# Kernel optimization log

Measured on AMD Instinct MI355X. Metric: run time of the kernel, lower is better.

Reference implementation:

```python
import jax, jax.numpy as jnp
import numpy as np

N_FEATURES = 512
FEATURE_DIM = 768
HIDDEN_DIM = 256


def setup_inputs() -> dict:
    key = jax.random.key(0)
    k0, k1, k2 = jax.random.split(key, 3)
    feature_embeddings = jax.random.normal(k0, (N_FEATURES, FEATURE_DIM), dtype=jnp.float32)
    # Linear(feature_dim*2 -> hidden) params, PyTorch-style init scale
    W1 = jax.random.normal(k1, (2 * FEATURE_DIM, HIDDEN_DIM), dtype=jnp.float32) / np.sqrt(2 * FEATURE_DIM)
    b1 = jnp.zeros((HIDDEN_DIM,), dtype=jnp.float32)
    W2 = jax.random.normal(k2, (HIDDEN_DIM, 1), dtype=jnp.float32) / np.sqrt(HIDDEN_DIM)
    b2 = jnp.zeros((1,), dtype=jnp.float32)
    return {"feature_embeddings": feature_embeddings, "W1": W1, "b1": b1, "W2": W2, "b2": b2}


def reference(feature_embeddings, W1, b1, W2, b2):
    n = feature_embeddings.shape[0]
    # all (i, j) with i < j -- same order as the original nested loop
    i_idx, j_idx = jnp.triu_indices(n, k=1)          # [P], [P]
    pairs = jnp.concatenate(
        [feature_embeddings[i_idx], feature_embeddings[j_idx]], axis=-1
    )                                                 # [P, 2*feature_dim]
    h = jax.nn.relu(pairs @ W1 + b1)                  # [P, hidden]
    scores = h @ W2 + b2                              # [P, 1]
    return i_idx, j_idx, scores
```

## Files before the change

### kernel.cpp

```cpp
#include <hip/hip_runtime.h>

#define FD 768
#define HD 256
#define NF 512
#define NC 512
#define PAIRS (NF * (NF - 1) / 2)

typedef __attribute__((ext_vector_type(4))) float f32x4;
typedef __attribute__((ext_vector_type(8))) short bf16x8;

__device__ inline unsigned bf16pk(float a, float b) {
    unsigned ua = __float_as_uint(a), ub = __float_as_uint(b);
    ua = (ua + 0x7FFFu + ((ua >> 16) & 1u)) >> 16;
    ub = (ub + 0x7FFFu + ((ub >> 16) & 1u)) >> 16;
    return ua | (ub << 16);
}

__global__ __launch_bounds__(256) void prep_kernel(
    const float* __restrict__ E, const float* __restrict__ W1,
    ushort* __restrict__ Ebf, ushort* __restrict__ Wt)
{
    const int bid = blockIdx.x, tid = threadIdx.x;
    if (bid < 384) {
        int idx = bid * 256 + tid;
        float4 v = ((const float4*)E)[idx];
        uint2 pk;
        pk.x = bf16pk(v.x, v.y);
        pk.y = bf16pk(v.z, v.w);
        *(uint2*)(Ebf + (size_t)idx * 4) = pk;
    } else {
        int t = (bid - 384) * 256 + tid;
        int q = t & 127, kp = t >> 7;
        int off = (q < 64) ? 0 : FD;
        int cq = q & 63;
        const float4* W14 = (const float4*)W1;
        float4 w0 = W14[(size_t)(2 * kp + off) * 64 + cq];
        float4 w1 = W14[(size_t)(2 * kp + 1 + off) * 64 + cq];
        *(unsigned*)(Wt + (size_t)(4 * q + 0) * FD + 2 * kp) = bf16pk(w0.x, w1.x);
        *(unsigned*)(Wt + (size_t)(4 * q + 1) * FD + 2 * kp) = bf16pk(w0.y, w1.y);
        *(unsigned*)(Wt + (size_t)(4 * q + 2) * FD + 2 * kp) = bf16pk(w0.z, w1.z);
        *(unsigned*)(Wt + (size_t)(4 * q + 3) * FD + 2 * kp) = bf16pk(w0.w, w1.w);
    }
}

__global__ __launch_bounds__(256) void gemm_mfma_kernel(
    const ushort* __restrict__ Ebf, const ushort* __restrict__ Wt,
    const float* __restrict__ b1, float* __restrict__ C)
{
    const int tid  = threadIdx.x;
    const int lane = tid & 63, wave = tid >> 6;
    const int wr = wave >> 1, wc = wave & 1;
    const int r0 = blockIdx.y * 32, c0 = blockIdx.x * 32;
    const int n = lane & 15, g = lane >> 4;

    const ushort* aptr = Wt  + (size_t)(c0 + 16 * wc + n) * FD + 8 * g;
    const ushort* bptr = Ebf + (size_t)(r0 + 16 * wr + n) * FD + 8 * g;

    f32x4 acc = {0.f, 0.f, 0.f, 0.f};
    #pragma unroll 8
    for (int ks = 0; ks < 24; ++ks) {
        bf16x8 af = *(const bf16x8*)(aptr + 32 * ks);
        bf16x8 bf = *(const bf16x8*)(bptr + 32 * ks);
        acc = __builtin_amdgcn_mfma_f32_16x16x32_bf16(af, bf, acc, 0, 0, 0);
    }

    const int row = r0 + 16 * wr + n;
    const int col = c0 + 16 * wc + 4 * g;
    float4 b = {0.f, 0.f, 0.f, 0.f};
    if (c0 < 256) b = ((const float4*)b1)[col >> 2];
    float4 o = {acc[0] + b.x, acc[1] + b.y, acc[2] + b.z, acc[3] + b.w};
    *(float4*)&C[(size_t)row * NC + col] = o;
}

__global__ __launch_bounds__(256) void pair_kernel(
    const float* __restrict__ C, const float* __restrict__ W2,
    const float* __restrict__ b2, float* __restrict__ out)
{
    __shared__ float4 As[16 * 64];
    __shared__ float4 Bs[32 * 64];

    int rem = blockIdx.x, bi = 0;
    while (rem >= 16 - (bi >> 1)) { rem -= 16 - (bi >> 1); ++bi; }
    const int bj = (bi >> 1) + rem;
    const int i0 = bi * 16, j0 = bj * 32;

    const int tid = threadIdx.x;
    const float4* C4 = (const float4*)C;

    #pragma unroll
    for (int s = 0; s < 4; ++s) {
        int idx = tid + 256 * s;
        int row = idx >> 6, c4 = idx & 63;
        As[row * 64 + (c4 ^ ((row >> 1) & 7))] = C4[(i0 + row) * 128 + c4];
    }
    #pragma unroll
    for (int s = 0; s < 8; ++s) {
        int idx = tid + 256 * s;
        int row = idx >> 6, c4 = idx & 63;
        Bs[row * 64 + (c4 ^ ((row >> 1) & 7))] = C4[(j0 + row) * 128 + 64 + c4];
    }
    __syncthreads();

    const int tx = tid & 15, ty = tid >> 4;
    const int keyA = (ty >> 1) & 7, keyB = tx & 7;
    const float4* W24 = (const float4*)W2;

    float acc0 = 0.f, acc1 = 0.f;
    #pragma unroll 8
    for (int k4 = 0; k4 < HD / 4; ++k4) {
        float4 a   = As[ty * 64 + (k4 ^ keyA)];
        float4 b0  = Bs[(2 * tx + 0) * 64 + (k4 ^ keyB)];
        float4 b1v = Bs[(2 * tx + 1) * 64 + (k4 ^ keyB)];
        float4 w = W24[k4];
        acc0 = fmaf(fmaxf(a.x + b0.x, 0.f), w.x, acc0);
        acc0 = fmaf(fmaxf(a.y + b0.y, 0.f), w.y, acc0);
        acc0 = fmaf(fmaxf(a.z + b0.z, 0.f), w.z, acc0);
        acc0 = fmaf(fmaxf(a.w + b0.w, 0.f), w.w, acc0);
        acc1 = fmaf(fmaxf(a.x + b1v.x, 0.f), w.x, acc1);
        acc1 = fmaf(fmaxf(a.y + b1v.y, 0.f), w.y, acc1);
        acc1 = fmaf(fmaxf(a.z + b1v.z, 0.f), w.z, acc1);
        acc1 = fmaf(fmaxf(a.w + b1v.w, 0.f), w.w, acc1);
    }

    const float bias2 = b2[0];
    const int i = i0 + ty;
    #pragma unroll
    for (int u = 0; u < 2; ++u) {
        int j = j0 + 2 * tx + u;
        float v = u ? acc1 : acc0;
        if (j > i) {
            int p = i * (2 * NF - i - 1) / 2 + (j - i - 1);
            out[p]             = (float)i;
            out[PAIRS + p]     = (float)j;
            out[2 * PAIRS + p] = v + bias2;
        }
    }
}

extern "C" void kernel_launch(void* const* d_in, const int* in_sizes, int n_in,
                              void* d_out, int out_size, void* d_ws, size_t ws_size,
                              hipStream_t stream) {
    const float* E  = (const float*)d_in[0];
    const float* W1 = (const float*)d_in[1];
    const float* b1 = (const float*)d_in[2];
    const float* W2 = (const float*)d_in[3];
    const float* b2 = (const float*)d_in[4];
    float* out = (float*)d_out;

    ushort* Ebf = (ushort*)d_ws;
    ushort* Wt  = Ebf + (size_t)NF * FD;
    float*  C   = (float*)((char*)d_ws + 2 * (size_t)NF * FD * 2);

    prep_kernel<<<576, 256, 0, stream>>>(E, W1, Ebf, Wt);
    gemm_mfma_kernel<<<dim3(16, 16), 256, 0, stream>>>(Ebf, Wt, b1, C);
    pair_kernel<<<272, 256, 0, stream>>>(C, W2, b2, out);
}
```

Baseline: 28.20 us.

## Transpose W1 via shared-memory tiles and compute 2x2 pairs per thread

The W1 transpose in the prep kernel now stages 64x64 tiles in padded shared memory, so both the global reads and the bf16 writes of the transposed weights are coalesced instead of strided. The pair kernel drops to 128 threads per block, each computing a 2x2 block of pair scores, which doubles register reuse of the A and B rows loaded from LDS. Fewer threads per block means less latency hiding and fewer waves per block across 272 blocks.

```diff
diff --git a/kernel.cpp b/kernel.cpp
--- a/kernel.cpp
+++ b/kernel.cpp
@@ -28,18 +28,40 @@
         pk.x = bf16pk(v.x, v.y);
         pk.y = bf16pk(v.z, v.w);
         *(uint2*)(Ebf + (size_t)idx * 4) = pk;
-    } else {
-        int t = (bid - 384) * 256 + tid;
-        int q = t & 127, kp = t >> 7;
-        int off = (q < 64) ? 0 : FD;
-        int cq = q & 63;
-        const float4* W14 = (const float4*)W1;
-        float4 w0 = W14[(size_t)(2 * kp + off) * 64 + cq];
-        float4 w1 = W14[(size_t)(2 * kp + 1 + off) * 64 + cq];
-        *(unsigned*)(Wt + (size_t)(4 * q + 0) * FD + 2 * kp) = bf16pk(w0.x, w1.x);
-        *(unsigned*)(Wt + (size_t)(4 * q + 1) * FD + 2 * kp) = bf16pk(w0.y, w1.y);
-        *(unsigned*)(Wt + (size_t)(4 * q + 2) * FD + 2 * kp) = bf16pk(w0.z, w1.z);
-        *(unsigned*)(Wt + (size_t)(4 * q + 3) * FD + 2 * kp) = bf16pk(w0.w, w1.w);
+        return;
+    }
+    __shared__ float Ls[64 * 65];
+    const int t = bid - 384;
+    const int kt = t % 12, rest = t / 12;
+    const int half = rest >> 3, ct = rest & 7;
+    const int k0 = kt * 64, c0 = ct * 64;
+    const int dofs = half ? FD : 0;
+
+    const float4* W14 = (const float4*)W1;
+    #pragma unroll
+    for (int s = 0; s < 4; ++s) {
+        int idx = tid + 256 * s;
+        int kr = idx >> 4, c4 = idx & 15;
+        float4 v = W14[(size_t)(dofs + k0 + kr) * 64 + (c0 >> 2) + c4];
+        Ls[kr * 65 + 4 * c4 + 0] = v.x;
+        Ls[kr * 65 + 4 * c4 + 1] = v.y;
+        Ls[kr * 65 + 4 * c4 + 2] = v.z;
+        Ls[kr * 65 + 4 * c4 + 3] = v.w;
+    }
+    __syncthreads();
+
+    const int kc = tid & 15, c_base = tid >> 4;
+    #pragma unroll
+    for (int s = 0; s < 4; ++s) {
+        int c_local = c_base + 16 * s;
+        float v0 = Ls[(4 * kc + 0) * 65 + c_local];
+        float v1 = Ls[(4 * kc + 1) * 65 + c_local];
+        float v2 = Ls[(4 * kc + 2) * 65 + c_local];
+        float v3 = Ls[(4 * kc + 3) * 65 + c_local];
+        uint2 pk;
+        pk.x = bf16pk(v0, v1);
+        pk.y = bf16pk(v2, v3);
+        *(uint2*)(Wt + (size_t)(half * 256 + c0 + c_local) * FD + k0 + 4 * kc) = pk;
     }
 }
 
@@ -72,7 +94,7 @@
     *(float4*)&C[(size_t)row * NC + col] = o;
 }
 
-__global__ __launch_bounds__(256) void pair_kernel(
+__global__ __launch_bounds__(128) void pair_kernel(
     const float* __restrict__ C, const float* __restrict__ W2,
     const float* __restrict__ b2, float* __restrict__ out)
 {
@@ -88,46 +110,47 @@
     const float4* C4 = (const float4*)C;
 
     #pragma unroll
-    for (int s = 0; s < 4; ++s) {
-        int idx = tid + 256 * s;
+    for (int s = 0; s < 8; ++s) {
+        int idx = tid + 128 * s;
         int row = idx >> 6, c4 = idx & 63;
         As[row * 64 + (c4 ^ ((row >> 1) & 7))] = C4[(i0 + row) * 128 + c4];
     }
     #pragma unroll
-    for (int s = 0; s < 8; ++s) {
-        int idx = tid + 256 * s;
+    for (int s = 0; s < 16; ++s) {
+        int idx = tid + 128 * s;
         int row = idx >> 6, c4 = idx & 63;
         Bs[row * 64 + (c4 ^ ((row >> 1) & 7))] = C4[(j0 + row) * 128 + 64 + c4];
     }
     __syncthreads();
 
     const int tx = tid & 15, ty = tid >> 4;
-    const int keyA = (ty >> 1) & 7, keyB = tx & 7;
+    const int ka = ty & 7, kb = tx & 7;
     const float4* W24 = (const float4*)W2;
 
-    float acc0 = 0.f, acc1 = 0.f;
+    float acc00 = 0.f, acc01 = 0.f, acc10 = 0.f, acc11 = 0.f;
     #pragma unroll 8
     for (int k4 = 0; k4 < HD / 4; ++k4) {
-        float4 a   = As[ty * 64 + (k4 ^ keyA)];
-        float4 b0  = Bs[(2 * tx + 0) * 64 + (k4 ^ keyB)];
-        float4 b1v = Bs[(2 * tx + 1) * 64 + (k4 ^ keyB)];
+        float4 a0  = As[(2 * ty + 0) * 64 + (k4 ^ ka)];
+        float4 a1  = As[(2 * ty + 1) * 64 + (k4 ^ ka)];
+        float4 b0  = Bs[(2 * tx + 0) * 64 + (k4 ^ kb)];
+        float4 b1v = Bs[(2 * tx + 1) * 64 + (k4 ^ kb)];
         float4 w = W24[k4];
-        acc0 = fmaf(fmaxf(a.x + b0.x, 0.f), w.x, acc0);
-        acc0 = fmaf(fmaxf(a.y + b0.y, 0.f), w.y, acc0);
-        acc0 = fmaf(fmaxf(a.z + b0.z, 0.f), w.z, acc0);
-        acc0 = fmaf(fmaxf(a.w + b0.w, 0.f), w.w, acc0);
-        acc1 = fmaf(fmaxf(a.x + b1v.x, 0.f), w.x, acc1);
-        acc1 = fmaf(fmaxf(a.y + b1v.y, 0.f), w.y, acc1);
-        acc1 = fmaf(fmaxf(a.z + b1v.z, 0.f), w.z, acc1);
-        acc1 = fmaf(fmaxf(a.w + b1v.w, 0.f), w.w, acc1);
+        #define PACC(ACC, A, B) \
+            ACC = fmaf(fmaxf(A.x + B.x, 0.f), w.x, ACC); \
+            ACC = fmaf(fmaxf(A.y + B.y, 0.f), w.y, ACC); \
+            ACC = fmaf(fmaxf(A.z + B.z, 0.f), w.z, ACC); \
+            ACC = fmaf(fmaxf(A.w + B.w, 0.f), w.w, ACC);
+        PACC(acc00, a0, b0) PACC(acc01, a0, b1v)
+        PACC(acc10, a1, b0) PACC(acc11, a1, b1v)
+        #undef PACC
     }
 
     const float bias2 = b2[0];
-    const int i = i0 + ty;
     #pragma unroll
-    for (int u = 0; u < 2; ++u) {
-        int j = j0 + 2 * tx + u;
-        float v = u ? acc1 : acc0;
+    for (int u = 0; u < 4; ++u) {
+        int i = i0 + 2 * ty + (u >> 1);
+        int j = j0 + 2 * tx + (u & 1);
+        float v = (u == 0) ? acc00 : (u == 1) ? acc01 : (u == 2) ? acc10 : acc11;
         if (j > i) {
             int p = i * (2 * NF - i - 1) / 2 + (j - i - 1);
             out[p]             = (float)i;
@@ -153,5 +176,5 @@
 
     prep_kernel<<<576, 256, 0, stream>>>(E, W1, Ebf, Wt);
     gemm_mfma_kernel<<<dim3(16, 16), 256, 0, stream>>>(Ebf, Wt, b1, C);
-    pair_kernel<<<272, 256, 0, stream>>>(C, W2, b2, out);
+    pair_kernel<<<272, 128, 0, stream>>>(C, W2, b2, out);
 }
```

Result: slower. 31.08 us (+10.2%).
